# Kernel tuning notes

Measured on AMD Instinct MI355X. Metric: run time of the kernel, lower is better.

The kernel has to match this reference:

```python
import jax, jax.numpy as jnp
import numpy as np

B, NG, GS, H = 256, 3008, 10, 6          # batch, n_genes, genes per leaf term, hidden per term
T = [2048, 256, 32, 1]                    # terms per DAG level (leaves -> root)
IN = [GS, 8 * H, 8 * H, 32 * H]           # per-term input size at each level
EPS = 1e-5


def setup_inputs() -> dict:
    keys = iter(jax.random.split(jax.random.key(0), 64))

    def rn(shape, s=0.1):
        return jax.random.normal(next(keys), shape, dtype=jnp.float32) * s

    d = {"x": rn((B, NG), 1.0),
         "gW": rn((T[0], GS, NG)),   # stacked leaf direct_gene_layer weights
         "gb": rn((T[0], GS))}
    for l in range(4):
        t, i = T[l], IN[l]
        d[f"w{l}"] = rn((t, H, i))          # term linear weight
        d[f"b{l}"] = rn((t, H))             # term linear bias
        d[f"g{l}"] = jnp.ones((t, H), jnp.float32)   # BN gamma
        d[f"e{l}"] = jnp.zeros((t, H), jnp.float32)  # BN beta
        d[f"p{l}"] = rn((t, H))             # aux linear1 weight (H->1)
        d[f"q{l}"] = rn((t,))               # aux linear1 bias
        d[f"r{l}"] = rn((t,))               # aux linear2 weight (1->1)
        d[f"s{l}"] = rn((t,))               # aux linear2 bias
    d["fw"] = rn((2 * H, H)); d["fb"] = rn((2 * H,))
    d["fg"] = jnp.ones((2 * H,), jnp.float32); d["fe"] = jnp.zeros((2 * H,), jnp.float32)
    d["pw"] = rn((1, 2 * H)); d["pb"] = rn((1,))
    d["rw"] = rn((1, 1)); d["rb"] = rn((1,))
    return d


def _bn(z, g, b):
    # BatchNorm1d in training mode: biased batch stats over axis 0
    m = z.mean(0)
    v = ((z - m) ** 2).mean(0)
    return (z - m) * jax.lax.rsqrt(v + EPS) * g + b


def reference(x, gW, gb,
              w0, b0, g0, e0, p0, q0, r0, s0,
              w1, b1, g1, e1, p1, q1, r1, s1,
              w2, b2, g2, e2, p2, q2, r2, s2,
              w3, b3, g3, e3, p3, q3, r3, s3,
              fw, fb, fg, fe, pw, pb, rw, rb):
    Bn = x.shape[0]
    # stacked direct gene layers for all leaf terms: [B, T0, GS]
    h = jnp.einsum('bn,tgn->btg', x, gW) + gb
    levels = [(w0, b0, g0, e0, p0, q0, r0, s0),
              (w1, b1, g1, e1, p1, q1, r1, s1),
              (w2, b2, g2, e2, p2, q2, r2, s2),
              (w3, b3, g3, e3, p3, q3, r3, s3)]
    aux = []
    for (w, b, g, e, p, q, r, s) in levels:
        # children of term t are contiguous -> concat == reshape
        hin = h.reshape(Bn, w.shape[0], w.shape[2])      # [B, T_l, in_l]
        z = jnp.tanh(jnp.einsum('bti,thi->bth', hin, w) + b)
        y = _bn(z, g, e)                                  # term_NN_out_map
        aux.append(r * jnp.tanh(jnp.einsum('bth,th->bt', y, p) + q) + s)
        h = y
    yroot = h.reshape(Bn, H)                              # root output [B, H]
    of = _bn(jnp.tanh(yroot @ fw.T + fb), fg, fe)         # final BN [B, 2H]
    auxf = jnp.tanh(of @ pw.T + pb) @ rw.T + rb           # final aux [B, 1]
    return jnp.concatenate(aux + [auxf], axis=1)          # [B, 2048+256+32+1+1]
```

## Files before the change

kernel.cpp:

```cpp
#include <hip/hip_runtime.h>
#include <hip/hip_bf16.h>
#include <stdint.h>

#define EPS 1e-5f
#define NOUT 2338

typedef __bf16 bf16x8 __attribute__((ext_vector_type(8)));
typedef float f32x4 __attribute__((ext_vector_type(4)));
typedef unsigned short u16;

__device__ __forceinline__ uint32_t pack2f(float lo, float hi) {
  union { __bf16 h[2]; uint32_t u; } r;
  r.h[0] = (__bf16)lo;
  r.h[1] = (__bf16)hi;
  return r.u;
}

__global__ __launch_bounds__(256) void cvt_pack_kernel(const float* __restrict__ x,
                                                       u16* __restrict__ xbp) {
  const int i = blockIdx.x * 256 + threadIdx.x;
  const int ks = i >> 10;
  const int rem = i & 1023;
  const int kb = rem >> 8;
  const int m = rem & 255;
  const f32x4* src = (const f32x4*)(x + (size_t)m * 3008 + ks * 32 + kb * 8);
  f32x4 a = src[0], b = src[1];
  uint4 o;
  o.x = pack2f(a.x, a.y);
  o.y = pack2f(a.z, a.w);
  o.z = pack2f(b.x, b.y);
  o.w = pack2f(b.z, b.w);
  ((uint4*)xbp)[i] = o;
}

__global__ __launch_bounds__(256, 4) void gemm_leaf(const float* __restrict__ W,
                                                    const float* __restrict__ gb,
                                                    const u16* __restrict__ XBp,
                                                    float* __restrict__ hout) {
  __shared__ __align__(16) u16 xl[2][8192];
  __shared__ __align__(16) u16 wl[2][2048];
  const int tid = threadIdx.x;
  const int w = tid >> 6;
  const int lane = tid & 63;
  const int rh = w >> 1;
  const int mh = w & 1;
  const int lquad = lane >> 4;
  const int lmod = lane & 15;
  const int n0 = (blockIdx.x >> 1) * 64;
  const int kh = blockIdx.x & 1;
  const int kbase = kh * 47;

  f32x4 acc[2][8];
#pragma unroll
  for (int a = 0; a < 2; ++a)
#pragma unroll
    for (int j = 0; j < 8; ++j) acc[a][j] = (f32x4){0.f, 0.f, 0.f, 0.f};

  const int wks = lane >> 4;
  const int wrl = lane & 15;
  const float* wgsrc = W + (size_t)(n0 + w * 16 + wrl) * 3008 + wks * 8;
  const int wdst = wks * 512 + (w * 16 + wrl) * 8;

#define STAGE_X(ks, buf)                                                                \
  do {                                                                                  \
    _Pragma("unroll")                                                                   \
    for (int p = 0; p < 4; ++p) {                                                       \
      const int c = (w * 4 + p) * 64;                                                   \
      const u16* src = XBp + (size_t)(ks) * 8192 + (size_t)(c + lane) * 8;              \
      u16* dst = &xl[buf][(size_t)c * 8];                                               \
      __builtin_amdgcn_global_load_lds((const __attribute__((address_space(1))) void*)src, \
                                       (__attribute__((address_space(3))) void*)dst,    \
                                       16, 0, 0);                                       \
    }                                                                                   \
  } while (0)

#define LOADW(ks, dA, dB)                                                               \
  do {                                                                                  \
    const f32x4* ap = (const f32x4*)(wgsrc + (size_t)(ks) * 32);                        \
    dA = ap[0];                                                                         \
    dB = ap[1];                                                                         \
  } while (0)

#define WRITEW(buf, dA, dB)                                                             \
  do {                                                                                  \
    union { uint32_t u[4]; bf16x8 v; } c;                                               \
    c.u[0] = pack2f(dA.x, dA.y);                                                        \
    c.u[1] = pack2f(dA.z, dA.w);                                                        \
    c.u[2] = pack2f(dB.x, dB.y);                                                        \
    c.u[3] = pack2f(dB.z, dB.w);                                                        \
    *(bf16x8*)(&wl[buf][wdst]) = c.v;                                                   \
  } while (0)

#define COMPUTE(buf)                                                                    \
  do {                                                                                  \
    const u16* xb = &xl[buf][(size_t)lquad * 2048 + mh * 1024 + lmod * 8];              \
    const u16* wb = &wl[buf][lquad * 512 + (rh * 32 + lmod) * 8];                       \
    const bf16x8 afA = *(const bf16x8*)(wb);                                            \
    const bf16x8 afB = *(const bf16x8*)(wb + 128);                        \
    _Pragma("unroll")                                                                   \
    for (int j = 0; j < 8; ++j) {                                                       \
      const bf16x8 bfrag = *(const bf16x8*)(xb + j * 128);                              \
      acc[0][j] = __builtin_amdgcn_mfma_f32_16x16x32_bf16(afA, bfrag, acc[0][j], 0, 0, 0); \
      acc[1][j] = __builtin_amdgcn_mfma_f32_16x16x32_bf16(afB, bfrag, acc[1][j], 0, 0, 0); \
    }                                                                                   \
  } while (0)

  {
    f32x4 wA, wB;
    LOADW(kbase, wA, wB);
    __builtin_amdgcn_sched_barrier(0);
    STAGE_X(kbase, 0);
    __builtin_amdgcn_sched_barrier(0);
    asm volatile("s_waitcnt vmcnt(4)" ::: "memory");
    __builtin_amdgcn_sched_barrier(0);
    WRITEW(0, wA, wB);
  }

  for (int s = 0; s < 47; ++s) {
    asm volatile("s_waitcnt vmcnt(0) lgkmcnt(0)" ::: "memory");
    __builtin_amdgcn_sched_barrier(0);
    __builtin_amdgcn_s_barrier();
    __builtin_amdgcn_sched_barrier(0);
    f32x4 nA = {0.f, 0.f, 0.f, 0.f}, nB = {0.f, 0.f, 0.f, 0.f};
    if (s < 46) LOADW(kbase + s + 1, nA, nB);
    __builtin_amdgcn_sched_barrier(0);
    if (s < 46) STAGE_X(kbase + s + 1, (s + 1) & 1);
    __builtin_amdgcn_sched_barrier(0);
    COMPUTE(s & 1);
    if (s < 46) {
      asm volatile("s_waitcnt vmcnt(4)" ::: "memory");
      __builtin_amdgcn_sched_barrier(0);
      WRITEW((s + 1) & 1, nA, nB);
    }
  }

#undef COMPUTE
#undef WRITEW
#undef LOADW
#undef STAGE_X

  float* hp = hout + (size_t)kh * 20480 * 256;
#pragma unroll
  for (int a = 0; a < 2; ++a) {
    const int r0 = n0 + rh * 32 + a * 16 + lquad * 4;
    float gb4[4];
#pragma unroll
    for (int r2 = 0; r2 < 4; ++r2) gb4[r2] = (kh == 0) ? gb[r0 + r2] : 0.f;
#pragma unroll
    for (int j = 0; j < 8; ++j) {
      const int col = (mh * 8 + j) * 16 + lmod;
#pragma unroll
      for (int r2 = 0; r2 < 4; ++r2) {
        hp[(size_t)(r0 + r2) * 256 + col] = acc[a][j][r2] + gb4[r2];
      }
    }
  }
}

__global__ __launch_bounds__(256) void level0_kernel(
    const float* __restrict__ yinA, const float* __restrict__ yinB,
    const float* __restrict__ w,
    const float* __restrict__ bia, const float* __restrict__ gam,
    const float* __restrict__ bet, const float* __restrict__ p,
    const float* __restrict__ q, const float* __restrict__ r,
    const float* __restrict__ s, float* __restrict__ yout,
    float* __restrict__ out, int inl, int off) {
  const int t = blockIdx.x;
  const int b = threadIdx.x;
  __shared__ float wls[6 * 10];
  __shared__ float part[4][12];
  __shared__ float stats[12];
  const float* wt = w + (size_t)t * 6 * inl;
  for (int i = b; i < 6 * inl; i += 256) wls[i] = wt[i];
  __syncthreads();

  float z[6];
#pragma unroll
  for (int h = 0; h < 6; ++h) z[h] = bia[t * 6 + h];
  const float* ypA = yinA + (size_t)t * inl * 256 + b;
  const float* ypB = yinB + (size_t)t * inl * 256 + b;
  for (int i = 0; i < inl; ++i) {
    float v = ypA[(size_t)i * 256] + ypB[(size_t)i * 256];
#pragma unroll
    for (int h = 0; h < 6; ++h) z[h] = fmaf(v, wls[h * inl + i], z[h]);
  }
#pragma unroll
  for (int h = 0; h < 6; ++h) z[h] = tanhf(z[h]);

  float sm[6], sq[6];
#pragma unroll
  for (int h = 0; h < 6; ++h) { sm[h] = z[h]; sq[h] = z[h] * z[h]; }
#pragma unroll
  for (int o = 32; o > 0; o >>= 1) {
#pragma unroll
    for (int h = 0; h < 6; ++h) {
      sm[h] += __shfl_down(sm[h], o);
      sq[h] += __shfl_down(sq[h], o);
    }
  }
  const int lane = b & 63, wvi = b >> 6;
  if (lane == 0) {
#pragma unroll
    for (int h = 0; h < 6; ++h) { part[wvi][h] = sm[h]; part[wvi][6 + h] = sq[h]; }
  }
  __syncthreads();
  if (b < 6) {
    float msum = part[0][b] + part[1][b] + part[2][b] + part[3][b];
    float qsum = part[0][6 + b] + part[1][6 + b] + part[2][6 + b] + part[3][6 + b];
    float m = msum * (1.f / 256.f);
    float var = qsum * (1.f / 256.f) - m * m;
    stats[b] = m;
    stats[6 + b] = rsqrtf(var + EPS);
  }
  __syncthreads();

  float a = q[t];
#pragma unroll
  for (int h = 0; h < 6; ++h) {
    float yy = (z[h] - stats[h]) * stats[6 + h] * gam[t * 6 + h] + bet[t * 6 + h];
    yout[((size_t)t * 6 + h) * 256 + b] = yy;
    a = fmaf(yy, p[t * 6 + h], a);
  }
  out[(size_t)b * NOUT + off + t] = tanhf(a) * r[t] + s[t];
}

__global__ __launch_bounds__(256) void level_kernel(
    const float* __restrict__ yin, const float* __restrict__ w,
    const float* __restrict__ bia, const float* __restrict__ gam,
    const float* __restrict__ bet, const float* __restrict__ p,
    const float* __restrict__ q, const float* __restrict__ r,
    const float* __restrict__ s, float* __restrict__ yout,
    float* __restrict__ out, int inl, int off) {
  const int t = blockIdx.x;
  const int b = threadIdx.x;
  __shared__ float wls[6 * 48];
  __shared__ float part[4][12];
  __shared__ float stats[12];
  const float* wt = w + (size_t)t * 6 * inl;
  for (int i = b; i < 6 * inl; i += 256) wls[i] = wt[i];
  __syncthreads();

  float z[6];
#pragma unroll
  for (int h = 0; h < 6; ++h) z[h] = bia[t * 6 + h];
  const float* yp = yin + (size_t)t * inl * 256 + b;
  for (int i = 0; i < inl; ++i) {
    float v = yp[(size_t)i * 256];
#pragma unroll
    for (int h = 0; h < 6; ++h) z[h] = fmaf(v, wls[h * inl + i], z[h]);
  }
#pragma unroll
  for (int h = 0; h < 6; ++h) z[h] = tanhf(z[h]);

  float sm[6], sq[6];
#pragma unroll
  for (int h = 0; h < 6; ++h) { sm[h] = z[h]; sq[h] = z[h] * z[h]; }
#pragma unroll
  for (int o = 32; o > 0; o >>= 1) {
#pragma unroll
    for (int h = 0; h < 6; ++h) {
      sm[h] += __shfl_down(sm[h], o);
      sq[h] += __shfl_down(sq[h], o);
    }
  }
  const int lane = b & 63, wvi = b >> 6;
  if (lane == 0) {
#pragma unroll
    for (int h = 0; h < 6; ++h) { part[wvi][h] = sm[h]; part[wvi][6 + h] = sq[h]; }
  }
  __syncthreads();
  if (b < 6) {
    float msum = part[0][b] + part[1][b] + part[2][b] + part[3][b];
    float qsum = part[0][6 + b] + part[1][6 + b] + part[2][6 + b] + part[3][6 + b];
    float m = msum * (1.f / 256.f);
    float var = qsum * (1.f / 256.f) - m * m;
    stats[b] = m;
    stats[6 + b] = rsqrtf(var + EPS);
  }
  __syncthreads();

  float a = q[t];
#pragma unroll
  for (int h = 0; h < 6; ++h) {
    float yy = (z[h] - stats[h]) * stats[6 + h] * gam[t * 6 + h] + bet[t * 6 + h];
    yout[((size_t)t * 6 + h) * 256 + b] = yy;
    a = fmaf(yy, p[t * 6 + h], a);
  }
  out[(size_t)b * NOUT + off + t] = tanhf(a) * r[t] + s[t];
}

__global__ __launch_bounds__(256) void level3_final_kernel(
    const float* __restrict__ y2,
    const float* __restrict__ w3, const float* __restrict__ b3,
    const float* __restrict__ g3, const float* __restrict__ e3,
    const float* __restrict__ p3, const float* __restrict__ q3,
    const float* __restrict__ r3, const float* __restrict__ s3,
    const float* __restrict__ fw, const float* __restrict__ fb,
    const float* __restrict__ fg, const float* __restrict__ fe,
    const float* __restrict__ pw, const float* __restrict__ pb,
    const float* __restrict__ rw, const float* __restrict__ rb,
    float* __restrict__ out) {
  const int b = threadIdx.x;
  __shared__ float wls[6 * 192];
  __shared__ float part[4][24];
  __shared__ float stats[24];
  for (int i = b; i < 6 * 192; i += 256) wls[i] = w3[i];
  __syncthreads();

  float z[6];
#pragma unroll
  for (int h = 0; h < 6; ++h) z[h] = b3[h];
  const float* yp = y2 + b;
  for (int i = 0; i < 192; ++i) {
    float v = yp[(size_t)i * 256];
#pragma unroll
    for (int h = 0; h < 6; ++h) z[h] = fmaf(v, wls[h * 192 + i], z[h]);
  }
#pragma unroll
  for (int h = 0; h < 6; ++h) z[h] = tanhf(z[h]);

  const int lane = b & 63, wvi = b >> 6;
  {
    float sm[6], sq[6];
#pragma unroll
    for (int h = 0; h < 6; ++h) { sm[h] = z[h]; sq[h] = z[h] * z[h]; }
#pragma unroll
    for (int o = 32; o > 0; o >>= 1) {
#pragma unroll
      for (int h = 0; h < 6; ++h) {
        sm[h] += __shfl_down(sm[h], o);
        sq[h] += __shfl_down(sq[h], o);
      }
    }
    if (lane == 0) {
#pragma unroll
      for (int h = 0; h < 6; ++h) { part[wvi][h] = sm[h]; part[wvi][6 + h] = sq[h]; }
    }
    __syncthreads();
    if (b < 6) {
      float msum = part[0][b] + part[1][b] + part[2][b] + part[3][b];
      float qsum = part[0][6 + b] + part[1][6 + b] + part[2][6 + b] + part[3][6 + b];
      float m = msum * (1.f / 256.f);
      float var = qsum * (1.f / 256.f) - m * m;
      stats[b] = m;
      stats[6 + b] = rsqrtf(var + EPS);
    }
    __syncthreads();
  }

  float yr[6];
  float a3 = q3[0];
#pragma unroll
  for (int h = 0; h < 6; ++h) {
    yr[h] = (z[h] - stats[h]) * stats[6 + h] * g3[h] + e3[h];
    a3 = fmaf(yr[h], p3[h], a3);
  }
  out[(size_t)b * NOUT + 2336] = tanhf(a3) * r3[0] + s3[0];
  __syncthreads();

  float zf[12];
#pragma unroll
  for (int j = 0; j < 12; ++j) {
    float a = fb[j];
#pragma unroll
    for (int h = 0; h < 6; ++h) a = fmaf(yr[h], fw[j * 6 + h], a);
    zf[j] = tanhf(a);
  }
  {
    float sm[12], sq[12];
#pragma unroll
    for (int j = 0; j < 12; ++j) { sm[j] = zf[j]; sq[j] = zf[j] * zf[j]; }
#pragma unroll
    for (int o = 32; o > 0; o >>= 1) {
#pragma unroll
      for (int j = 0; j < 12; ++j) {
        sm[j] += __shfl_down(sm[j], o);
        sq[j] += __shfl_down(sq[j], o);
      }
    }
    if (lane == 0) {
#pragma unroll
      for (int j = 0; j < 12; ++j) { part[wvi][j] = sm[j]; part[wvi][12 + j] = sq[j]; }
    }
    __syncthreads();
    if (b < 12) {
      float msum = part[0][b] + part[1][b] + part[2][b] + part[3][b];
      float qsum = part[0][12 + b] + part[1][12 + b] + part[2][12 + b] + part[3][12 + b];
      float m = msum * (1.f / 256.f);
      float var = qsum * (1.f / 256.f) - m * m;
      stats[b] = m;
      stats[12 + b] = rsqrtf(var + EPS);
    }
    __syncthreads();
  }
  float a = pb[0];
#pragma unroll
  for (int j = 0; j < 12; ++j) {
    float of = (zf[j] - stats[j]) * stats[12 + j] * fg[j] + fe[j];
    a = fmaf(of, pw[j], a);
  }
  out[(size_t)b * NOUT + 2337] = tanhf(a) * rw[0] + rb[0];
}

extern "C" void kernel_launch(void* const* d_in, const int* in_sizes, int n_in,
                              void* d_out, int out_size, void* d_ws, size_t ws_size,
                              hipStream_t stream) {
  const float* x  = (const float*)d_in[0];
  const float* gW = (const float*)d_in[1];
  const float* gb = (const float*)d_in[2];
  float* out = (float*)d_out;

  char* wsb = (char*)d_ws;
  u16* XBp = (u16*)wsb;
  float* h0 = (float*)(wsb + 1540096);
  float* y0 = h0 + (size_t)2 * 20480 * 256;
  float* y1 = y0 + (size_t)12288 * 256;
  float* y2 = y1 + (size_t)1536 * 256;

  cvt_pack_kernel<<<dim3(376), dim3(256), 0, stream>>>(x, XBp);
  gemm_leaf<<<dim3(640), dim3(256), 0, stream>>>(gW, gb, XBp, h0);

  level0_kernel<<<dim3(2048), dim3(256), 0, stream>>>(
      h0, h0 + (size_t)20480 * 256,
      (const float*)d_in[3], (const float*)d_in[4], (const float*)d_in[5],
      (const float*)d_in[6], (const float*)d_in[7], (const float*)d_in[8],
      (const float*)d_in[9], (const float*)d_in[10], y0, out, 10, 0);

#define LV(base, yin, yout, inl, off, grid)                                           \
  level_kernel<<<dim3(grid), dim3(256), 0, stream>>>(                                 \
      yin, (const float*)d_in[base], (const float*)d_in[base + 1],                    \
      (const float*)d_in[base + 2], (const float*)d_in[base + 3],                     \
      (const float*)d_in[base + 4], (const float*)d_in[base + 5],                     \
      (const float*)d_in[base + 6], (const float*)d_in[base + 7], yout, out, inl, off)

  LV(11, y0, y1, 48,  2048, 256);
  LV(19, y1, y2, 48,  2304, 32);
#undef LV

  level3_final_kernel<<<dim3(1), dim3(256), 0, stream>>>(
      y2,
      (const float*)d_in[27], (const float*)d_in[28], (const float*)d_in[29],
      (const float*)d_in[30], (const float*)d_in[31], (const float*)d_in[32],
      (const float*)d_in[33], (const float*)d_in[34],
      (const float*)d_in[35], (const float*)d_in[36], (const float*)d_in[37],
      (const float*)d_in[38], (const float*)d_in[39], (const float*)d_in[40],
      (const float*)d_in[41], (const float*)d_in[42], out);
}
```

Before: 155.2 us.

## Widen leaf GEMM tile to 128 rows with 4-way split-K and swizzled weight LDS

The leaf GEMM block now covers 128 output rows instead of 64, with four accumulator fragments per wave, so each staged X tile is reused across twice as many weight rows. The K dimension is split four ways (24/24/23/23 steps) instead of two, keeping the grid at 640 blocks, and the level-0 kernel sums four partial buffers. The weight LDS layout is XOR-swizzled to avoid bank conflicts, and the loop barrier becomes __syncthreads. The costs are more accumulator registers (occupancy hint lowered to 3), twice the partial-output traffic, and a larger workspace.

```diff
diff --git a/kernel.cpp b/kernel.cpp
--- a/kernel.cpp
+++ b/kernel.cpp
@@ -33,12 +33,12 @@
   ((uint4*)xbp)[i] = o;
 }
 
-__global__ __launch_bounds__(256, 4) void gemm_leaf(const float* __restrict__ W,
+__global__ __launch_bounds__(256, 3) void gemm_leaf(const float* __restrict__ W,
                                                     const float* __restrict__ gb,
                                                     const u16* __restrict__ XBp,
                                                     float* __restrict__ hout) {
   __shared__ __align__(16) u16 xl[2][8192];
-  __shared__ __align__(16) u16 wl[2][2048];
+  __shared__ __align__(16) u16 wl[2][4096];
   const int tid = threadIdx.x;
   const int w = tid >> 6;
   const int lane = tid & 63;
@@ -46,20 +46,16 @@
   const int mh = w & 1;
   const int lquad = lane >> 4;
   const int lmod = lane & 15;
-  const int n0 = (blockIdx.x >> 1) * 64;
-  const int kh = blockIdx.x & 1;
-  const int kbase = kh * 47;
-
-  f32x4 acc[2][8];
-#pragma unroll
-  for (int a = 0; a < 2; ++a)
+  const int n0 = (blockIdx.x >> 2) * 128;
+  const int kh = blockIdx.x & 3;
+  const int kbase = kh * 24 - ((kh > 2) ? (kh - 2) : 0);
+  const int nst = 24 - ((kh >= 2) ? 1 : 0);
+
+  f32x4 acc[4][8];
+#pragma unroll
+  for (int a = 0; a < 4; ++a)
 #pragma unroll
     for (int j = 0; j < 8; ++j) acc[a][j] = (f32x4){0.f, 0.f, 0.f, 0.f};
-
-  const int wks = lane >> 4;
-  const int wrl = lane & 15;
-  const float* wgsrc = W + (size_t)(n0 + w * 16 + wrl) * 3008 + wks * 8;
-  const int wdst = wks * 512 + (w * 16 + wrl) * 8;
 
 #define STAGE_X(ks, buf)                                                                \
   do {                                                                                  \
@@ -74,63 +70,76 @@
     }                                                                                   \
   } while (0)
 
-#define LOADW(ks, dA, dB)                                                               \
+  const int wks = lane >> 4;
+  const int wrl = lane & 15;
+  const int wrow0 = w * 32 + wrl;
+  const int wrow1 = wrow0 + 16;
+  const float* wg0 = W + (size_t)(n0 + wrow0) * 3008 + wks * 8;
+  const float* wg1 = W + (size_t)(n0 + wrow1) * 3008 + wks * 8;
+  const int wo0 = wrow0 * 32 + ((wks ^ (wrow0 & 3)) * 8);
+  const int wo1 = wrow1 * 32 + ((wks ^ (wrow1 & 3)) * 8);
+
+#define LOADW(ks, dA0, dA1, dB0, dB1)                                                   \
   do {                                                                                  \
-    const f32x4* ap = (const f32x4*)(wgsrc + (size_t)(ks) * 32);                        \
-    dA = ap[0];                                                                         \
-    dB = ap[1];                                                                         \
+    const f32x4* a0 = (const f32x4*)(wg0 + (size_t)(ks) * 32);                          \
+    dA0 = a0[0]; dA1 = a0[1];                                                           \
+    const f32x4* a1 = (const f32x4*)(wg1 + (size_t)(ks) * 32);                          \
+    dB0 = a1[0]; dB1 = a1[1];                                                           \
   } while (0)
 
-#define WRITEW(buf, dA, dB)                                                             \
+#define WRITEW(buf, dA0, dA1, dB0, dB1)                                                 \
   do {                                                                                  \
-    union { uint32_t u[4]; bf16x8 v; } c;                                               \
-    c.u[0] = pack2f(dA.x, dA.y);                                                        \
-    c.u[1] = pack2f(dA.z, dA.w);                                                        \
-    c.u[2] = pack2f(dB.x, dB.y);                                                        \
-    c.u[3] = pack2f(dB.z, dB.w);                                                        \
-    *(bf16x8*)(&wl[buf][wdst]) = c.v;                                                   \
+    union { uint32_t u[4]; bf16x8 v; } c0, c1;                                          \
+    c0.u[0] = pack2f(dA0.x, dA0.y); c0.u[1] = pack2f(dA0.z, dA0.w);                     \
+    c0.u[2] = pack2f(dA1.x, dA1.y); c0.u[3] = pack2f(dA1.z, dA1.w);                     \
+    c1.u[0] = pack2f(dB0.x, dB0.y); c1.u[1] = pack2f(dB0.z, dB0.w);                     \
+    c1.u[2] = pack2f(dB1.x, dB1.y); c1.u[3] = pack2f(dB1.z, dB1.w);                     \
+    *(bf16x8*)(&wl[buf][wo0]) = c0.v;                                                   \
+    *(bf16x8*)(&wl[buf][wo1]) = c1.v;                                                   \
   } while (0)
 
 #define COMPUTE(buf)                                                                    \
   do {                                                                                  \
     const u16* xb = &xl[buf][(size_t)lquad * 2048 + mh * 1024 + lmod * 8];              \
-    const u16* wb = &wl[buf][lquad * 512 + (rh * 32 + lmod) * 8];                       \
-    const bf16x8 afA = *(const bf16x8*)(wb);                                            \
-    const bf16x8 afB = *(const bf16x8*)(wb + 128);                        \
+    bf16x8 af[4];                                                                       \
+    _Pragma("unroll")                                                                   \
+    for (int a = 0; a < 4; ++a) {                                                       \
+      const int row = rh * 64 + a * 16 + lmod;                                          \
+      af[a] = *(const bf16x8*)(&wl[buf][row * 32 + ((lquad ^ (row & 3)) * 8)]);         \
+    }                                                                                   \
     _Pragma("unroll")                                                                   \
     for (int j = 0; j < 8; ++j) {                                                       \
       const bf16x8 bfrag = *(const bf16x8*)(xb + j * 128);                              \
-      acc[0][j] = __builtin_amdgcn_mfma_f32_16x16x32_bf16(afA, bfrag, acc[0][j], 0, 0, 0); \
-      acc[1][j] = __builtin_amdgcn_mfma_f32_16x16x32_bf16(afB, bfrag, acc[1][j], 0, 0, 0); \
+      acc[0][j] = __builtin_amdgcn_mfma_f32_16x16x32_bf16(af[0], bfrag, acc[0][j], 0, 0, 0); \
+      acc[1][j] = __builtin_amdgcn_mfma_f32_16x16x32_bf16(af[1], bfrag, acc[1][j], 0, 0, 0); \
+      acc[2][j] = __builtin_amdgcn_mfma_f32_16x16x32_bf16(af[2], bfrag, acc[2][j], 0, 0, 0); \
+      acc[3][j] = __builtin_amdgcn_mfma_f32_16x16x32_bf16(af[3], bfrag, acc[3][j], 0, 0, 0); \
     }                                                                                   \
   } while (0)
 
   {
-    f32x4 wA, wB;
-    LOADW(kbase, wA, wB);
+    f32x4 wA0, wA1, wB0, wB1;
+    LOADW(kbase, wA0, wA1, wB0, wB1);
     __builtin_amdgcn_sched_barrier(0);
     STAGE_X(kbase, 0);
     __builtin_amdgcn_sched_barrier(0);
     asm volatile("s_waitcnt vmcnt(4)" ::: "memory");
     __builtin_amdgcn_sched_barrier(0);
-    WRITEW(0, wA, wB);
-  }
-
-  for (int s = 0; s < 47; ++s) {
-    asm volatile("s_waitcnt vmcnt(0) lgkmcnt(0)" ::: "memory");
+    WRITEW(0, wA0, wA1, wB0, wB1);
+  }
+
+  for (int s = 0; s < nst; ++s) {
+    __syncthreads();
+    f32x4 nA0 = {0,0,0,0}, nA1 = {0,0,0,0}, nB0 = {0,0,0,0}, nB1 = {0,0,0,0};
+    if (s + 1 < nst) LOADW(kbase + s + 1, nA0, nA1, nB0, nB1);
     __builtin_amdgcn_sched_barrier(0);
-    __builtin_amdgcn_s_barrier();
-    __builtin_amdgcn_sched_barrier(0);
-    f32x4 nA = {0.f, 0.f, 0.f, 0.f}, nB = {0.f, 0.f, 0.f, 0.f};
-    if (s < 46) LOADW(kbase + s + 1, nA, nB);
-    __builtin_amdgcn_sched_barrier(0);
-    if (s < 46) STAGE_X(kbase + s + 1, (s + 1) & 1);
+    if (s + 1 < nst) STAGE_X(kbase + s + 1, (s + 1) & 1);
     __builtin_amdgcn_sched_barrier(0);
     COMPUTE(s & 1);
-    if (s < 46) {
+    if (s + 1 < nst) {
       asm volatile("s_waitcnt vmcnt(4)" ::: "memory");
       __builtin_amdgcn_sched_barrier(0);
-      WRITEW((s + 1) & 1, nA, nB);
+      WRITEW((s + 1) & 1, nA0, nA1, nB0, nB1);
     }
   }
 
@@ -141,8 +150,8 @@
 
   float* hp = hout + (size_t)kh * 20480 * 256;
 #pragma unroll
-  for (int a = 0; a < 2; ++a) {
-    const int r0 = n0 + rh * 32 + a * 16 + lquad * 4;
+  for (int a = 0; a < 4; ++a) {
+    const int r0 = n0 + rh * 64 + a * 16 + lquad * 4;
     float gb4[4];
 #pragma unroll
     for (int r2 = 0; r2 < 4; ++r2) gb4[r2] = (kh == 0) ? gb[r0 + r2] : 0.f;
@@ -158,8 +167,7 @@
 }
 
 __global__ __launch_bounds__(256) void level0_kernel(
-    const float* __restrict__ yinA, const float* __restrict__ yinB,
-    const float* __restrict__ w,
+    const float* __restrict__ yin, const float* __restrict__ w,
     const float* __restrict__ bia, const float* __restrict__ gam,
     const float* __restrict__ bet, const float* __restrict__ p,
     const float* __restrict__ q, const float* __restrict__ r,
@@ -167,6 +175,7 @@
     float* __restrict__ out, int inl, int off) {
   const int t = blockIdx.x;
   const int b = threadIdx.x;
+  const size_t P = (size_t)20480 * 256;
   __shared__ float wls[6 * 10];
   __shared__ float part[4][12];
   __shared__ float stats[12];
@@ -177,10 +186,10 @@
   float z[6];
 #pragma unroll
   for (int h = 0; h < 6; ++h) z[h] = bia[t * 6 + h];
-  const float* ypA = yinA + (size_t)t * inl * 256 + b;
-  const float* ypB = yinB + (size_t)t * inl * 256 + b;
+  const float* yp = yin + (size_t)t * inl * 256 + b;
   for (int i = 0; i < inl; ++i) {
-    float v = ypA[(size_t)i * 256] + ypB[(size_t)i * 256];
+    const size_t o = (size_t)i * 256;
+    float v = yp[o] + yp[P + o] + yp[2 * P + o] + yp[3 * P + o];
 #pragma unroll
     for (int h = 0; h < 6; ++h) z[h] = fmaf(v, wls[h * inl + i], z[h]);
   }
@@ -413,7 +422,7 @@
   char* wsb = (char*)d_ws;
   u16* XBp = (u16*)wsb;
   float* h0 = (float*)(wsb + 1540096);
-  float* y0 = h0 + (size_t)2 * 20480 * 256;
+  float* y0 = h0 + (size_t)4 * 20480 * 256;
   float* y1 = y0 + (size_t)12288 * 256;
   float* y2 = y1 + (size_t)1536 * 256;
 
@@ -421,7 +430,7 @@
   gemm_leaf<<<dim3(640), dim3(256), 0, stream>>>(gW, gb, XBp, h0);
 
   level0_kernel<<<dim3(2048), dim3(256), 0, stream>>>(
-      h0, h0 + (size_t)20480 * 256,
+      h0,
       (const float*)d_in[3], (const float*)d_in[4], (const float*)d_in[5],
       (const float*)d_in[6], (const float*)d_in[7], (const float*)d_in[8],
       (const float*)d_in[9], (const float*)d_in[10], y0, out, 10, 0);
```

Result: slower. 259.6 us (+67.2%).
